# Optimization experiments

Hardware: AMD Instinct MI355X
Metric: run time of the kernel (lower is better)

Reference implementation:

```python
import jax, jax.numpy as jnp
import numpy as np

D_MODEL = 128
DEPTH = 4
LN_EPS = 1e-5


def _ssm(x, Wi, A, Wo):
    # x: [B, L, D]; Wi: [3D, D]; A: [D]; Wo: [D, D]
    z = jnp.einsum('bld,ed->ble', x, Wi)          # [B, L, 3D]
    u, i, o = jnp.split(z, 3, axis=-1)
    iu = jax.nn.sigmoid(i) * jnp.tanh(u)          # gated input, [B, L, D]
    og = jax.nn.sigmoid(o)                        # output gate
    a = jnp.minimum(jnp.exp(A), 0.999)            # decay, [D]

    def step(s, c):
        s = a * s + c
        return s, s

    s0 = jnp.zeros((x.shape[0], x.shape[2]), x.dtype)
    _, S = jax.lax.scan(step, s0, jnp.swapaxes(iu, 0, 1))  # [L, B, D]
    y = og * jnp.swapaxes(S, 0, 1)                # [B, L, D]
    return jnp.einsum('bld,ed->ble', y, Wo)


def _scan_2d(x, Wi, A, Wo):
    # x: [N, D, H, W] -> four directional 1D scans, averaged
    N, D, H, W = x.shape
    xh = jnp.transpose(x, (0, 2, 3, 1))           # [N, H, W, D]
    lr = _ssm(xh.reshape(N * H, W, D), Wi, A, Wo).reshape(N, H, W, D)
    rl = _ssm(jnp.flip(xh, 2).reshape(N * H, W, D), Wi, A, Wo).reshape(N, H, W, D)
    rl = jnp.flip(rl, 2)
    xw = jnp.transpose(x, (0, 3, 2, 1))           # [N, W, H, D]
    ud = _ssm(xw.reshape(N * W, H, D), Wi, A, Wo).reshape(N, W, H, D)
    du = _ssm(jnp.flip(xw, 2).reshape(N * W, H, D), Wi, A, Wo).reshape(N, W, H, D)
    du = jnp.flip(du, 2)
    y = (lr + rl + jnp.transpose(ud, (0, 2, 1, 3)) + jnp.transpose(du, (0, 2, 1, 3))) / 4
    return jnp.transpose(y, (0, 3, 1, 2))         # [N, D, H, W]


def setup_inputs() -> dict:
    key = jax.random.key(0)
    ks = jax.random.split(key, 8)
    D = D_MODEL
    lin = 1.0 / np.sqrt(D)
    tok = jax.random.normal(ks[0], (8, 16, D, 32, 32), jnp.float32)
    s_inp = jax.random.normal(ks[1], (DEPTH, 3 * D, D), jnp.float32) * lin
    s_A = jax.random.normal(ks[2], (DEPTH, D), jnp.float32) * -0.1
    s_out = jax.random.normal(ks[3], (DEPTH, D, D), jnp.float32) * lin
    t_inp = jax.random.normal(ks[4], (DEPTH, 3 * D, D), jnp.float32) * lin
    t_A = jax.random.normal(ks[5], (DEPTH, D), jnp.float32) * -0.1
    t_out = jax.random.normal(ks[6], (DEPTH, D, D), jnp.float32) * lin
    ln_g = jnp.ones((D,), jnp.float32)
    ln_b = jnp.zeros((D,), jnp.float32)
    return {"tok": tok, "s_inp": s_inp, "s_A": s_A, "s_out": s_out,
            "t_inp": t_inp, "t_A": t_A, "t_out": t_out,
            "ln_g": ln_g, "ln_b": ln_b}


def reference(tok, s_inp, s_A, s_out, t_inp, t_A, t_out, ln_g, ln_b):
    B, T, D, h, w = tok.shape
    x = tok
    for l in range(DEPTH):
        xs = x.reshape(B * T, D, h, w)
        xs = _scan_2d(xs, s_inp[l], s_A[l], s_out[l]).reshape(B, T, D, h, w)
        xt = jnp.transpose(xs, (0, 3, 4, 1, 2)).reshape(B * h * w, T, D)
        xt = _ssm(xt, t_inp[l], t_A[l], t_out[l]).reshape(B, h, w, T, D)
        x = x + jnp.transpose(xt, (0, 3, 4, 1, 2))
    xn = jnp.transpose(x, (0, 1, 3, 4, 2))        # [B,T,h,w,D]
    mu = jnp.mean(xn, axis=-1, keepdims=True)
    var = jnp.var(xn, axis=-1, keepdims=True)
    xn = (xn - mu) / jnp.sqrt(var + LN_EPS) * ln_g + ln_b
    return jnp.transpose(xn, (0, 1, 4, 2, 3))     # [B,T,D,h,w]
```

## Files before the change

kernel.cpp:

```cpp
#include <hip/hip_runtime.h>
#include <hip/hip_bf16.h>
#include <math.h>

#define D_MODEL 128
#define HW      1024
#define DEPTH   4
#define NIMG    128
#define B_      8
#define T_      16
#define LN_EPSF 1e-5f
#define TLN     131072
#define PS      1033

typedef short  s8  __attribute__((ext_vector_type(8)));
typedef ushort us8 __attribute__((ext_vector_type(8)));
typedef ushort us4 __attribute__((ext_vector_type(4)));
typedef float  f4  __attribute__((ext_vector_type(4)));

#define MFMA __builtin_amdgcn_mfma_f32_16x16x32_bf16

__device__ __forceinline__ float sig_(float x) { return 1.0f / (1.0f + __expf(-x)); }
__device__ __forceinline__ float tanh_(float x) { return 2.0f * sig_(2.0f * x) - 1.0f; }
__device__ __forceinline__ ushort f2b(float f) {
    __hip_bfloat16 h = __float2bfloat16(f);
    return *reinterpret_cast<ushort*>(&h);
}
__device__ __forceinline__ float b2f(ushort u) {
    __hip_bfloat16 h = *reinterpret_cast<__hip_bfloat16*>(&u);
    return __bfloat162float(h);
}

__global__ __launch_bounds__(256) void wconv_kernel(
    const float* __restrict__ src, ushort* __restrict__ dst, int n)
{
    int i = blockIdx.x * 256 + threadIdx.x;
    if (i < n) dst[i] = f2b(src[i]);
}

__device__ __forceinline__ void gates_from_lds_TL(
    const ushort (*Xs)[136], const ushort* __restrict__ Wi,
    ushort* __restrict__ iu, ushort* __restrict__ og,
    size_t nbase, int q0, int tid)
{
    const int lane = tid & 63, wv = tid >> 6, grp = lane >> 4, lrow = lane & 15;
    const int ch0 = wv * 32;

    {
        f4 aU[2][4], aI[2][4];
        #pragma unroll
        for (int nt = 0; nt < 2; ++nt)
            #pragma unroll
            for (int qt = 0; qt < 4; ++qt) { aU[nt][qt] = (f4)0.f; aI[nt][qt] = (f4)0.f; }

        #pragma unroll
        for (int kk = 0; kk < 4; ++kk) {
            const int kb = kk * 32 + grp * 8;
            s8 xb[4], wu[2], wi[2];
            #pragma unroll
            for (int qt = 0; qt < 4; ++qt)
                xb[qt] = *reinterpret_cast<const s8*>(&Xs[qt * 16 + lrow][kb]);
            #pragma unroll
            for (int nt = 0; nt < 2; ++nt) {
                const int e = ch0 + nt * 16 + lrow;
                wu[nt] = *reinterpret_cast<const s8*>(Wi + (size_t)e * D_MODEL + kb);
                wi[nt] = *reinterpret_cast<const s8*>(Wi + (size_t)(e + 128) * D_MODEL + kb);
            }
            #pragma unroll
            for (int nt = 0; nt < 2; ++nt)
                #pragma unroll
                for (int qt = 0; qt < 4; ++qt) {
                    aU[nt][qt] = MFMA(wu[nt], xb[qt], aU[nt][qt], 0, 0, 0);
                    aI[nt][qt] = MFMA(wi[nt], xb[qt], aI[nt][qt], 0, 0, 0);
                }
        }
        #pragma unroll
        for (int nt = 0; nt < 2; ++nt)
            #pragma unroll
            for (int qt = 0; qt < 4; ++qt) {
                const int ch = ch0 + nt * 16 + grp * 4;
                const int q  = q0 + qt * 16 + lrow;
                const size_t off = nbase + (size_t)(ch >> 3) * 8192 + (size_t)q * 8 + (ch & 7);
                us4 piu;
                #pragma unroll
                for (int i = 0; i < 4; ++i)
                    piu[i] = f2b(sig_(aI[nt][qt][i]) * tanh_(aU[nt][qt][i]));
                *reinterpret_cast<us4*>(iu + off) = piu;
            }
    }

    {
        f4 aO[2][4];
        #pragma unroll
        for (int nt = 0; nt < 2; ++nt)
            #pragma unroll
            for (int qt = 0; qt < 4; ++qt) aO[nt][qt] = (f4)0.f;

        #pragma unroll
        for (int kk = 0; kk < 4; ++kk) {
            const int kb = kk * 32 + grp * 8;
            s8 xb[4], wo[2];
            #pragma unroll
            for (int qt = 0; qt < 4; ++qt)
                xb[qt] = *reinterpret_cast<const s8*>(&Xs[qt * 16 + lrow][kb]);
            #pragma unroll
            for (int nt = 0; nt < 2; ++nt)
                wo[nt] = *reinterpret_cast<const s8*>(Wi + (size_t)(ch0 + nt * 16 + lrow + 256) * D_MODEL + kb);
            #pragma unroll
            for (int nt = 0; nt < 2; ++nt)
                #pragma unroll
                for (int qt = 0; qt < 4; ++qt)
                    aO[nt][qt] = MFMA(wo[nt], xb[qt], aO[nt][qt], 0, 0, 0);
        }
        #pragma unroll
        for (int nt = 0; nt < 2; ++nt)
            #pragma unroll
            for (int qt = 0; qt < 4; ++qt) {
                const int ch = ch0 + nt * 16 + grp * 4;
                const int q  = q0 + qt * 16 + lrow;
                const size_t off = nbase + (size_t)(ch >> 3) * 8192 + (size_t)q * 8 + (ch & 7);
                us4 pog;
                #pragma unroll
                for (int i = 0; i < 4; ++i)
                    pog[i] = f2b(sig_(aO[nt][qt][i]));
                *reinterpret_cast<us4*>(og + off) = pog;
            }
    }
}

__global__ __launch_bounds__(256, 3) void gates_f32_kernel(
    const float* __restrict__ in, const ushort* __restrict__ Wi,
    ushort* __restrict__ iu, ushort* __restrict__ og)
{
    __shared__ ushort Xs[64][136];
    const int n   = blockIdx.x >> 4;
    const int q0  = (blockIdx.x & 15) << 6;
    const int tid = threadIdx.x;
    const size_t nbase = (size_t)n * TLN;

    {
        const float* inb = in + nbase + q0;
        const int q = tid & 63, dh0 = tid >> 6;
        for (int it = 0; it < 4; ++it) {
            const int dh = dh0 + it * 4;
            s8 pk;
            #pragma unroll
            for (int j = 0; j < 8; ++j)
                pk[j] = (short)f2b(inb[(size_t)(dh * 8 + j) * HW + q]);
            *reinterpret_cast<s8*>(&Xs[q][dh * 8]) = pk;
        }
    }
    __syncthreads();
    gates_from_lds_TL(Xs, Wi, iu, og, nbase, q0, tid);
}

__global__ __launch_bounds__(256, 2) void scan2d_kernel(
    ushort* bufG , const ushort* __restrict__ og,
    const float* __restrict__ Av)
{
    __shared__ float P[8 * PS];
    __shared__ float R[8 * PS];
    const int n   = blockIdx.x >> 4;
    const int oct = blockIdx.x & 15;
    const int tid = threadIdx.x;
    const size_t base = (size_t)n * TLN + (size_t)oct * 8192;

    for (int it = 0; it < 4; ++it) {
        const int p  = it * 256 + tid;
        const int sw = p ^ (((p >> 5) & 7) << 2);
        us8 v = *reinterpret_cast<const us8*>(bufG + base + (size_t)p * 8);
        #pragma unroll
        for (int dc = 0; dc < 8; ++dc) P[dc * PS + sw] = b2f(v[dc]);
    }
    __syncthreads();

    const int dc  = tid & 7;
    const int row = tid >> 3;
    const float a = fminf(__expf(Av[oct * 8 + dc]), 0.999f);

    {
        const int swb = (row * 32) ^ (((row & 7) << 2));
        float x[32], r[32];
        #pragma unroll
        for (int j = 0; j < 32; ++j) x[j] = P[dc * PS + (swb ^ j)];
        float s = 0.f;
        #pragma unroll
        for (int j = 0; j < 32; ++j) { s = fmaf(a, s, x[j]); r[j] = s; }
        s = 0.f;
        #pragma unroll
        for (int j = 31; j >= 0; --j) { s = fmaf(a, s, x[j]); r[j] += s; }
        #pragma unroll
        for (int j = 0; j < 32; ++j) R[dc * PS + (swb ^ j)] = r[j];
    }
    __syncthreads();

    {
        float x[32], t[32];
        #pragma unroll
        for (int i = 0; i < 32; ++i) {
            const int p = i * 32 + row;
            x[i] = P[dc * PS + (p ^ ((i & 7) << 2))];
        }
        float s = 0.f;
        #pragma unroll
        for (int i = 0; i < 32; ++i) { s = fmaf(a, s, x[i]); t[i] = s; }
        s = 0.f;
        #pragma unroll
        for (int i = 31; i >= 0; --i) { s = fmaf(a, s, x[i]); t[i] += s; }
        #pragma unroll
        for (int i = 0; i < 32; ++i) {
            const int idx = dc * PS + ((i * 32 + row) ^ ((i & 7) << 2));
            P[idx] = t[i] + R[idx];
        }
    }
    __syncthreads();

    for (int it = 0; it < 4; ++it) {
        const int p  = it * 256 + tid;
        const int sw = p ^ (((p >> 5) & 7) << 2);
        us8 o = *reinterpret_cast<const us8*>(og + base + (size_t)p * 8);
        us8 w;
        #pragma unroll
        for (int d2 = 0; d2 < 8; ++d2)
            w[d2] = f2b(b2f(o[d2]) * P[d2 * PS + sw] * 0.25f);
        *reinterpret_cast<us8*>(bufG + base + (size_t)p * 8) = w;
    }
}

__global__ __launch_bounds__(256, 3) void fusedA_kernel(
    ushort* bufA , ushort* bufB ,
    const ushort* __restrict__ WoS, const ushort* __restrict__ WiT)
{
    __shared__ ushort Xs[64][136];
    const int n   = blockIdx.x >> 4;
    const int q0  = (blockIdx.x & 15) << 6;
    const int tid = threadIdx.x;
    const int lane = tid & 63, wv = tid >> 6, grp = lane >> 4, lrow = lane & 15;
    const size_t nbase = (size_t)n * TLN;
    const int qq = q0 + wv * 16 + lrow;

    s8 gf[4];
    #pragma unroll
    for (int kk = 0; kk < 4; ++kk)
        gf[kk] = *reinterpret_cast<const s8*>(
            bufA + nbase + (size_t)(kk * 4 + grp) * 8192 + (size_t)qq * 8);

    f4 C[8];
    #pragma unroll
    for (int et = 0; et < 8; ++et) C[et] = (f4)0.f;
    #pragma unroll
    for (int kk = 0; kk < 4; ++kk) {
        const int kb = kk * 32 + grp * 8;
        #pragma unroll
        for (int et = 0; et < 8; ++et) {
            s8 wf = *reinterpret_cast<const s8*>(WoS + (size_t)(et * 16 + lrow) * D_MODEL + kb);
            C[et] = MFMA(gf[kk], wf, C[et], 0, 0, 0);
        }
    }

    #pragma unroll
    for (int et = 0; et < 8; ++et)
        #pragma unroll
        for (int i = 0; i < 4; ++i)
            Xs[wv * 16 + grp * 4 + i][et * 16 + lrow] = f2b(C[et][i]);
    __syncthreads();

    gates_from_lds_TL(Xs, WiT, bufA, bufB, nbase, q0, tid);
}

__global__ __launch_bounds__(256) void tscan_kernel(
    ushort* __restrict__ buf, const float* __restrict__ Av)
{
    const int tid = blockIdx.x * 256 + threadIdx.x;
    const int q   = tid & 1023;
    const int oct = (tid >> 10) & 15;
    const int b   = tid >> 14;
    float aa[8], st[8];
    #pragma unroll
    for (int jj = 0; jj < 8; ++jj) {
        aa[jj] = fminf(__expf(Av[oct * 8 + jj]), 0.999f);
        st[jj] = 0.f;
    }
    const size_t base = (size_t)(b * T_) * TLN + (size_t)oct * 8192 + (size_t)q * 8;
    #pragma unroll
    for (int t = 0; t < T_; ++t) {
        ushort* p = buf + base + (size_t)t * TLN;
        us8 v = *reinterpret_cast<us8*>(p);
        us8 w;
        #pragma unroll
        for (int jj = 0; jj < 8; ++jj) {
            st[jj] = fmaf(aa[jj], st[jj], b2f(v[jj]));
            w[jj] = f2b(st[jj]);
        }
        *reinterpret_cast<us8*>(p) = w;
    }
}

template <bool GATES, bool LN>
__global__ __launch_bounds__(256, 3) void fusedB_kernel(
    ushort* bufA , ushort* bufB ,
    const ushort* __restrict__ WoT, const float* __restrict__ resid,
    float* __restrict__ X, const ushort* __restrict__ WiS2,
    const float* __restrict__ lng, const float* __restrict__ lnb)
{
    __shared__ ushort Xs[64][136];
    const int n   = blockIdx.x >> 4;
    const int q0  = (blockIdx.x & 15) << 6;
    const int tid = threadIdx.x;
    const int lane = tid & 63, wv = tid >> 6, grp = lane >> 4, lrow = lane & 15;
    const size_t nbase = (size_t)n * TLN;
    const int qq = q0 + wv * 16 + lrow;

    s8 g[4];
    #pragma unroll
    for (int kk = 0; kk < 4; ++kk) {
        const size_t off = nbase + (size_t)(kk * 4 + grp) * 8192 + (size_t)qq * 8;
        us8 sv = *reinterpret_cast<const us8*>(bufA + off);
        us8 ov = *reinterpret_cast<const us8*>(bufB + off);
        s8 gg;
        #pragma unroll
        for (int j = 0; j < 8; ++j)
            gg[j] = (short)f2b(b2f(sv[j]) * b2f(ov[j]));
        g[kk] = gg;
    }

    f4 C[8];
    #pragma unroll
    for (int et = 0; et < 8; ++et) C[et] = (f4)0.f;
    #pragma unroll
    for (int kk = 0; kk < 4; ++kk) {
        const int kb = kk * 32 + grp * 8;
        #pragma unroll
        for (int et = 0; et < 8; ++et) {
            s8 wf = *reinterpret_cast<const s8*>(WoT + (size_t)(et * 16 + lrow) * D_MODEL + kb);
            C[et] = MFMA(g[kk], wf, C[et], 0, 0, 0);
        }
    }

    const int qb = q0 + wv * 16 + grp * 4;

    #pragma unroll
    for (int et = 0; et < 8; ++et) {
        const int e = et * 16 + lrow;
        const size_t offR = nbase + (size_t)e * HW + qb;
        f4 r = *reinterpret_cast<const f4*>(resid + offR);
        #pragma unroll
        for (int i = 0; i < 4; ++i) C[et][i] += r[i];
    }

    if constexpr (LN) {
        float s4[4] = {0.f,0.f,0.f,0.f}, q4[4] = {0.f,0.f,0.f,0.f};
        #pragma unroll
        for (int et = 0; et < 8; ++et)
            #pragma unroll
            for (int i = 0; i < 4; ++i) {
                s4[i] += C[et][i];
                q4[i] += C[et][i] * C[et][i];
            }
        #pragma unroll
        for (int m = 1; m <= 8; m <<= 1)
            #pragma unroll
            for (int i = 0; i < 4; ++i) {
                s4[i] += __shfl_xor(s4[i], m);
                q4[i] += __shfl_xor(q4[i], m);
            }
        float mean[4], rstd[4];
        #pragma unroll
        for (int i = 0; i < 4; ++i) {
            mean[i] = s4[i] * (1.f / D_MODEL);
            rstd[i] = rsqrtf(q4[i] * (1.f / D_MODEL) - mean[i] * mean[i] + LN_EPSF);
        }
        #pragma unroll
        for (int et = 0; et < 8; ++et) {
            const int e = et * 16 + lrow;
            const float ge = lng[e], be = lnb[e];
            const size_t offX = nbase + (size_t)e * HW + qb;
            f4 o;
            #pragma unroll
            for (int i = 0; i < 4; ++i)
                o[i] = (C[et][i] - mean[i]) * rstd[i] * ge + be;
            *reinterpret_cast<f4*>(X + offX) = o;
        }
    } else {
        #pragma unroll
        for (int et = 0; et < 8; ++et) {
            const int e = et * 16 + lrow;
            const size_t offX = nbase + (size_t)e * HW + qb;
            f4 v;
            #pragma unroll
            for (int i = 0; i < 4; ++i) v[i] = C[et][i];
            *reinterpret_cast<f4*>(X + offX) = v;
            if constexpr (GATES) {
                #pragma unroll
                for (int i = 0; i < 4; ++i)
                    Xs[wv * 16 + grp * 4 + i][e] = f2b(v[i]);
            }
        }
        if constexpr (GATES) {
            __syncthreads();
            gates_from_lds_TL(Xs, WiS2, bufA, bufB, nbase, q0, tid);
        }
    }
}

extern "C" void kernel_launch(void* const* d_in, const int* in_sizes, int n_in,
                              void* d_out, int out_size, void* d_ws, size_t ws_size,
                              hipStream_t stream) {
    const float* tok   = (const float*)d_in[0];
    const float* s_inp = (const float*)d_in[1];
    const float* s_A   = (const float*)d_in[2];
    const float* s_out = (const float*)d_in[3];
    const float* t_inp = (const float*)d_in[4];
    const float* t_A   = (const float*)d_in[5];
    const float* t_out = (const float*)d_in[6];
    const float* ln_g  = (const float*)d_in[7];
    const float* ln_b  = (const float*)d_in[8];

    float*  X    = (float*)d_out;
    ushort* Abuf = (ushort*)d_ws;
    ushort* Bbuf = Abuf + (size_t)16777216;
    ushort* Wbf  = Bbuf + (size_t)16777216;
    ushort* sWiB = Wbf;
    ushort* sWoB = Wbf + 196608;
    ushort* tWiB = Wbf + 262144;
    ushort* tWoB = Wbf + 458752;

    const dim3 blk256(256);

    wconv_kernel<<<768, blk256, 0, stream>>>(s_inp, sWiB, 196608);
    wconv_kernel<<<256, blk256, 0, stream>>>(s_out, sWoB, 65536);
    wconv_kernel<<<768, blk256, 0, stream>>>(t_inp, tWiB, 196608);
    wconv_kernel<<<256, blk256, 0, stream>>>(t_out, tWoB, 65536);

    gates_f32_kernel<<<2048, blk256, 0, stream>>>(tok, sWiB, Abuf, Bbuf);

    for (int l = 0; l < DEPTH; ++l) {
        const float* xin = (l == 0) ? tok : X;

        scan2d_kernel<<<2048, blk256, 0, stream>>>(Abuf, Bbuf, s_A + (size_t)l * 128);
        fusedA_kernel<<<2048, blk256, 0, stream>>>(
            Abuf, Bbuf, sWoB + (size_t)l * 16384, tWiB + (size_t)l * 49152);
        tscan_kernel<<<512, blk256, 0, stream>>>(Abuf, t_A + (size_t)l * 128);

        if (l < DEPTH - 1) {
            fusedB_kernel<true, false><<<2048, blk256, 0, stream>>>(
                Abuf, Bbuf, tWoB + (size_t)l * 16384, xin, X,
                sWiB + (size_t)(l + 1) * 49152, nullptr, nullptr);
        } else {
            fusedB_kernel<false, true><<<2048, blk256, 0, stream>>>(
                Abuf, Bbuf, tWoB + (size_t)l * 16384, xin, X,
                nullptr, ln_g, ln_b);
        }
    }
}
```

Measured before the change: 764.3 us.

## Switch intermediate gate buffers from channel-octet to channel-major layout

Changes the bf16 intermediate buffers from an [oct][q][8] interleaved layout to plain channel-major [D][HW]. All producers and consumers (gate GEMMs, 2D scan, time scan, fused output kernels) are rewritten to transpose through LDS with the new indexing, and the MFMA operand order is swapped to match. The scan kernel now prefetches the output gate before filling LDS, and the fused-B kernel is split into a residual-plus-gates version and a separate layernorm version. The aim is more contiguous global accesses and simpler time-scan addressing. The cost is extra LDS transposes, with possible bank conflicts on column-wise writes.

Result: faster. 683.1 us, median of 2 (-10.6%).

```diff
diff --git a/kernel.cpp b/kernel.cpp
--- a/kernel.cpp
+++ b/kernel.cpp
@@ -37,7 +37,7 @@
     if (i < n) dst[i] = f2b(src[i]);
 }
 
-__device__ __forceinline__ void gates_from_lds_TL(
+__device__ __forceinline__ void gates_from_lds(
     const ushort (*Xs)[136], const ushort* __restrict__ Wi,
     ushort* __restrict__ iu, ushort* __restrict__ og,
     size_t nbase, int q0, int tid)
@@ -46,19 +46,19 @@
     const int ch0 = wv * 32;
 
     {
-        f4 aU[2][4], aI[2][4];
-        #pragma unroll
-        for (int nt = 0; nt < 2; ++nt)
-            #pragma unroll
-            for (int qt = 0; qt < 4; ++qt) { aU[nt][qt] = (f4)0.f; aI[nt][qt] = (f4)0.f; }
+        f4 aU[4][2], aI[4][2];
+        #pragma unroll
+        for (int mt = 0; mt < 4; ++mt)
+            #pragma unroll
+            for (int nt = 0; nt < 2; ++nt) { aU[mt][nt] = (f4)0.f; aI[mt][nt] = (f4)0.f; }
 
         #pragma unroll
         for (int kk = 0; kk < 4; ++kk) {
             const int kb = kk * 32 + grp * 8;
-            s8 xb[4], wu[2], wi[2];
-            #pragma unroll
-            for (int qt = 0; qt < 4; ++qt)
-                xb[qt] = *reinterpret_cast<const s8*>(&Xs[qt * 16 + lrow][kb]);
+            s8 xa[4], wu[2], wi[2];
+            #pragma unroll
+            for (int mt = 0; mt < 4; ++mt)
+                xa[mt] = *reinterpret_cast<const s8*>(&Xs[mt * 16 + lrow][kb]);
             #pragma unroll
             for (int nt = 0; nt < 2; ++nt) {
                 const int e = ch0 + nt * 16 + lrow;
@@ -66,62 +66,59 @@
                 wi[nt] = *reinterpret_cast<const s8*>(Wi + (size_t)(e + 128) * D_MODEL + kb);
             }
             #pragma unroll
-            for (int nt = 0; nt < 2; ++nt)
+            for (int mt = 0; mt < 4; ++mt)
                 #pragma unroll
-                for (int qt = 0; qt < 4; ++qt) {
-                    aU[nt][qt] = MFMA(wu[nt], xb[qt], aU[nt][qt], 0, 0, 0);
-                    aI[nt][qt] = MFMA(wi[nt], xb[qt], aI[nt][qt], 0, 0, 0);
+                for (int nt = 0; nt < 2; ++nt) {
+                    aU[mt][nt] = MFMA(xa[mt], wu[nt], aU[mt][nt], 0, 0, 0);
+                    aI[mt][nt] = MFMA(xa[mt], wi[nt], aI[mt][nt], 0, 0, 0);
                 }
         }
         #pragma unroll
-        for (int nt = 0; nt < 2; ++nt)
-            #pragma unroll
-            for (int qt = 0; qt < 4; ++qt) {
-                const int ch = ch0 + nt * 16 + grp * 4;
-                const int q  = q0 + qt * 16 + lrow;
-                const size_t off = nbase + (size_t)(ch >> 3) * 8192 + (size_t)q * 8 + (ch & 7);
+        for (int mt = 0; mt < 4; ++mt)
+            #pragma unroll
+            for (int nt = 0; nt < 2; ++nt) {
+                const int e = ch0 + nt * 16 + lrow;
+                const size_t off = nbase + (size_t)e * HW + q0 + mt * 16 + grp * 4;
                 us4 piu;
                 #pragma unroll
                 for (int i = 0; i < 4; ++i)
-                    piu[i] = f2b(sig_(aI[nt][qt][i]) * tanh_(aU[nt][qt][i]));
+                    piu[i] = f2b(sig_(aI[mt][nt][i]) * tanh_(aU[mt][nt][i]));
                 *reinterpret_cast<us4*>(iu + off) = piu;
             }
     }
-
     {
-        f4 aO[2][4];
-        #pragma unroll
-        for (int nt = 0; nt < 2; ++nt)
-            #pragma unroll
-            for (int qt = 0; qt < 4; ++qt) aO[nt][qt] = (f4)0.f;
+        f4 aO[4][2];
+        #pragma unroll
+        for (int mt = 0; mt < 4; ++mt)
+            #pragma unroll
+            for (int nt = 0; nt < 2; ++nt) aO[mt][nt] = (f4)0.f;
 
         #pragma unroll
         for (int kk = 0; kk < 4; ++kk) {
             const int kb = kk * 32 + grp * 8;
-            s8 xb[4], wo[2];
-            #pragma unroll
-            for (int qt = 0; qt < 4; ++qt)
-                xb[qt] = *reinterpret_cast<const s8*>(&Xs[qt * 16 + lrow][kb]);
+            s8 xa[4], wo[2];
+            #pragma unroll
+            for (int mt = 0; mt < 4; ++mt)
+                xa[mt] = *reinterpret_cast<const s8*>(&Xs[mt * 16 + lrow][kb]);
             #pragma unroll
             for (int nt = 0; nt < 2; ++nt)
                 wo[nt] = *reinterpret_cast<const s8*>(Wi + (size_t)(ch0 + nt * 16 + lrow + 256) * D_MODEL + kb);
             #pragma unroll
-            for (int nt = 0; nt < 2; ++nt)
+            for (int mt = 0; mt < 4; ++mt)
                 #pragma unroll
-                for (int qt = 0; qt < 4; ++qt)
-                    aO[nt][qt] = MFMA(wo[nt], xb[qt], aO[nt][qt], 0, 0, 0);
-        }
-        #pragma unroll
-        for (int nt = 0; nt < 2; ++nt)
-            #pragma unroll
-            for (int qt = 0; qt < 4; ++qt) {
-                const int ch = ch0 + nt * 16 + grp * 4;
-                const int q  = q0 + qt * 16 + lrow;
-                const size_t off = nbase + (size_t)(ch >> 3) * 8192 + (size_t)q * 8 + (ch & 7);
+                for (int nt = 0; nt < 2; ++nt)
+                    aO[mt][nt] = MFMA(xa[mt], wo[nt], aO[mt][nt], 0, 0, 0);
+        }
+        #pragma unroll
+        for (int mt = 0; mt < 4; ++mt)
+            #pragma unroll
+            for (int nt = 0; nt < 2; ++nt) {
+                const int e = ch0 + nt * 16 + lrow;
+                const size_t off = nbase + (size_t)e * HW + q0 + mt * 16 + grp * 4;
                 us4 pog;
                 #pragma unroll
                 for (int i = 0; i < 4; ++i)
-                    pog[i] = f2b(sig_(aO[nt][qt][i]));
+                    pog[i] = f2b(sig_(aO[mt][nt][i]));
                 *reinterpret_cast<us4*>(og + off) = pog;
             }
     }
@@ -137,20 +134,17 @@
     const int tid = threadIdx.x;
     const size_t nbase = (size_t)n * TLN;
 
-    {
-        const float* inb = in + nbase + q0;
-        const int q = tid & 63, dh0 = tid >> 6;
-        for (int it = 0; it < 4; ++it) {
-            const int dh = dh0 + it * 4;
-            s8 pk;
-            #pragma unroll
-            for (int j = 0; j < 8; ++j)
-                pk[j] = (short)f2b(inb[(size_t)(dh * 8 + j) * HW + q]);
-            *reinterpret_cast<s8*>(&Xs[q][dh * 8]) = pk;
-        }
-    }
-    __syncthreads();
-    gates_from_lds_TL(Xs, Wi, iu, og, nbase, q0, tid);
+    #pragma unroll
+    for (int it = 0; it < 8; ++it) {
+        const int c  = it * 256 + tid;
+        const int ch = c >> 4;
+        const int qo = c & 15;
+        f4 v = *reinterpret_cast<const f4*>(in + nbase + (size_t)ch * HW + q0 + qo * 4);
+        #pragma unroll
+        for (int j = 0; j < 4; ++j) Xs[qo * 4 + j][ch] = f2b(v[j]);
+    }
+    __syncthreads();
+    gates_from_lds(Xs, Wi, iu, og, nbase, q0, tid);
 }
 
 __global__ __launch_bounds__(256, 2) void scan2d_kernel(
@@ -162,14 +156,26 @@
     const int n   = blockIdx.x >> 4;
     const int oct = blockIdx.x & 15;
     const int tid = threadIdx.x;
-    const size_t base = (size_t)n * TLN + (size_t)oct * 8192;
-
+    const size_t base = (size_t)n * TLN + (size_t)(oct * 8) * HW;
+
+    us8 ogv[4];
+    #pragma unroll
     for (int it = 0; it < 4; ++it) {
-        const int p  = it * 256 + tid;
-        const int sw = p ^ (((p >> 5) & 7) << 2);
-        us8 v = *reinterpret_cast<const us8*>(bufG + base + (size_t)p * 8);
-        #pragma unroll
-        for (int dc = 0; dc < 8; ++dc) P[dc * PS + sw] = b2f(v[dc]);
+        const int c  = it * 256 + tid;
+        const int dc = c >> 7, po = c & 127;
+        ogv[it] = *reinterpret_cast<const us8*>(og + base + (size_t)dc * HW + po * 8);
+    }
+
+    #pragma unroll
+    for (int it = 0; it < 4; ++it) {
+        const int c  = it * 256 + tid;
+        const int dc = c >> 7, po = c & 127;
+        us8 v = *reinterpret_cast<const us8*>(bufG + base + (size_t)dc * HW + po * 8);
+        #pragma unroll
+        for (int j = 0; j < 8; ++j) {
+            const int p = po * 8 + j;
+            P[dc * PS + (p ^ (((p >> 5) & 7) << 2))] = b2f(v[j]);
+        }
     }
     __syncthreads();
 
@@ -178,7 +184,7 @@
     const float a = fminf(__expf(Av[oct * 8 + dc]), 0.999f);
 
     {
-        const int swb = (row * 32) ^ (((row & 7) << 2));
+        const int swb = (row * 32) ^ ((row & 7) << 2);
         float x[32], r[32];
         #pragma unroll
         for (int j = 0; j < 32; ++j) x[j] = P[dc * PS + (swb ^ j)];
@@ -214,15 +220,17 @@
     }
     __syncthreads();
 
+    #pragma unroll
     for (int it = 0; it < 4; ++it) {
-        const int p  = it * 256 + tid;
-        const int sw = p ^ (((p >> 5) & 7) << 2);
-        us8 o = *reinterpret_cast<const us8*>(og + base + (size_t)p * 8);
+        const int c  = it * 256 + tid;
+        const int dc2 = c >> 7, po = c & 127;
         us8 w;
         #pragma unroll
-        for (int d2 = 0; d2 < 8; ++d2)
-            w[d2] = f2b(b2f(o[d2]) * P[d2 * PS + sw] * 0.25f);
-        *reinterpret_cast<us8*>(bufG + base + (size_t)p * 8) = w;
+        for (int j = 0; j < 8; ++j) {
+            const int p = po * 8 + j;
+            w[j] = f2b(b2f(ogv[it][j]) * P[dc2 * PS + (p ^ (((p >> 5) & 7) << 2))] * 0.25f);
+        }
+        *reinterpret_cast<us8*>(bufG + base + (size_t)dc2 * HW + po * 8) = w;
     }
 }
 
@@ -230,19 +238,194 @@
     ushort* bufA , ushort* bufB ,
     const ushort* __restrict__ WoS, const ushort* __restrict__ WiT)
 {
-    __shared__ ushort Xs[64][136];
+    __shared__ ushort Gs[64][136];
+    const int n   = blockIdx.x >> 4;
+    const int q0  = (blockIdx.x & 15) << 6;
+    const int tid = threadIdx.x;
+    const int lane = tid & 63, wv = tid >> 6, grp = lane >> 4, lrow = lane & 15;
+    const int ch0 = wv * 32;
+    const size_t nbase = (size_t)n * TLN;
+
+    #pragma unroll
+    for (int it = 0; it < 4; ++it) {
+        const int c  = it * 256 + tid;
+        const int ch = c >> 3, qo = c & 7;
+        us8 v = *reinterpret_cast<const us8*>(bufA + nbase + (size_t)ch * HW + q0 + qo * 8);
+        #pragma unroll
+        for (int j = 0; j < 8; ++j) Gs[qo * 8 + j][ch] = v[j];
+    }
+    __syncthreads();
+
+    f4 c1[2][4];
+    #pragma unroll
+    for (int et = 0; et < 2; ++et)
+        #pragma unroll
+        for (int qt = 0; qt < 4; ++qt) c1[et][qt] = (f4)0.f;
+
+    #pragma unroll
+    for (int kk = 0; kk < 4; ++kk) {
+        const int kb = kk * 32 + grp * 8;
+        s8 wf[2], xg[4];
+        #pragma unroll
+        for (int et = 0; et < 2; ++et)
+            wf[et] = *reinterpret_cast<const s8*>(WoS + (size_t)(ch0 + et * 16 + lrow) * D_MODEL + kb);
+        #pragma unroll
+        for (int qt = 0; qt < 4; ++qt)
+            xg[qt] = *reinterpret_cast<const s8*>(&Gs[qt * 16 + lrow][kb]);
+        #pragma unroll
+        for (int et = 0; et < 2; ++et)
+            #pragma unroll
+            for (int qt = 0; qt < 4; ++qt)
+                c1[et][qt] = MFMA(wf[et], xg[qt], c1[et][qt], 0, 0, 0);
+    }
+    __syncthreads();
+
+    #pragma unroll
+    for (int et = 0; et < 2; ++et)
+        #pragma unroll
+        for (int qt = 0; qt < 4; ++qt) {
+            us4 pk;
+            #pragma unroll
+            for (int i = 0; i < 4; ++i) pk[i] = f2b(c1[et][qt][i]);
+            *reinterpret_cast<us4*>(&Gs[qt * 16 + lrow][ch0 + et * 16 + grp * 4]) = pk;
+        }
+    __syncthreads();
+
+    gates_from_lds(Gs, WiT, bufA, bufB, nbase, q0, tid);
+}
+
+__global__ __launch_bounds__(256) void tscan_kernel(
+    ushort* __restrict__ buf, const float* __restrict__ Av)
+{
+    const int tid = blockIdx.x * 256 + threadIdx.x;
+    const int qo = tid & 127;
+    const int d  = (tid >> 7) & 127;
+    const int b  = tid >> 14;
+    const float a = fminf(__expf(Av[d]), 0.999f);
+    const size_t base = (size_t)(b * T_) * TLN + (size_t)d * HW + qo * 8;
+    float st[8];
+    #pragma unroll
+    for (int j = 0; j < 8; ++j) st[j] = 0.f;
+    #pragma unroll
+    for (int t = 0; t < T_; ++t) {
+        ushort* p = buf + base + (size_t)t * TLN;
+        us8 v = *reinterpret_cast<us8*>(p);
+        us8 w;
+        #pragma unroll
+        for (int j = 0; j < 8; ++j) {
+            st[j] = fmaf(a, st[j], b2f(v[j]));
+            w[j] = f2b(st[j]);
+        }
+        *reinterpret_cast<us8*>(p) = w;
+    }
+}
+
+__global__ __launch_bounds__(256, 3) void fusedB_kernel(
+    ushort* bufA , ushort* bufB ,
+    const ushort* __restrict__ WoT, const float* __restrict__ resid,
+    float* __restrict__ X, const ushort* __restrict__ WiS2)
+{
+    __shared__ ushort Gs[64][136];
+    const int n   = blockIdx.x >> 4;
+    const int q0  = (blockIdx.x & 15) << 6;
+    const int tid = threadIdx.x;
+    const int lane = tid & 63, wv = tid >> 6, grp = lane >> 4, lrow = lane & 15;
+    const int ch0 = wv * 32;
+    const size_t nbase = (size_t)n * TLN;
+
+    #pragma unroll
+    for (int it = 0; it < 4; ++it) {
+        const int c  = it * 256 + tid;
+        const int ch = c >> 3, qo = c & 7;
+        const size_t o = nbase + (size_t)ch * HW + q0 + qo * 8;
+        us8 sv = *reinterpret_cast<const us8*>(bufA + o);
+        us8 ov = *reinterpret_cast<const us8*>(bufB + o);
+        #pragma unroll
+        for (int j = 0; j < 8; ++j) Gs[qo * 8 + j][ch] = f2b(b2f(sv[j]) * b2f(ov[j]));
+    }
+
+    f4 r[4][2];
+    #pragma unroll
+    for (int mt = 0; mt < 4; ++mt)
+        #pragma unroll
+        for (int nt = 0; nt < 2; ++nt)
+            r[mt][nt] = *reinterpret_cast<const f4*>(
+                resid + nbase + (size_t)(ch0 + nt * 16 + lrow) * HW + q0 + mt * 16 + grp * 4);
+    __syncthreads();
+
+    f4 C[4][2];
+    #pragma unroll
+    for (int mt = 0; mt < 4; ++mt)
+        #pragma unroll
+        for (int nt = 0; nt < 2; ++nt) C[mt][nt] = (f4)0.f;
+
+    #pragma unroll
+    for (int kk = 0; kk < 4; ++kk) {
+        const int kb = kk * 32 + grp * 8;
+        s8 xg[4], wf[2];
+        #pragma unroll
+        for (int mt = 0; mt < 4; ++mt)
+            xg[mt] = *reinterpret_cast<const s8*>(&Gs[mt * 16 + lrow][kb]);
+        #pragma unroll
+        for (int nt = 0; nt < 2; ++nt)
+            wf[nt] = *reinterpret_cast<const s8*>(WoT + (size_t)(ch0 + nt * 16 + lrow) * D_MODEL + kb);
+        #pragma unroll
+        for (int mt = 0; mt < 4; ++mt)
+            #pragma unroll
+            for (int nt = 0; nt < 2; ++nt)
+                C[mt][nt] = MFMA(xg[mt], wf[nt], C[mt][nt], 0, 0, 0);
+    }
+    __syncthreads();
+
+    #pragma unroll
+    for (int mt = 0; mt < 4; ++mt)
+        #pragma unroll
+        for (int nt = 0; nt < 2; ++nt) {
+            const int e    = ch0 + nt * 16 + lrow;
+            const int qloc = mt * 16 + grp * 4;
+            const size_t off = nbase + (size_t)e * HW + q0 + qloc;
+            f4 v;
+            #pragma unroll
+            for (int i = 0; i < 4; ++i) v[i] = C[mt][nt][i] + r[mt][nt][i];
+            *reinterpret_cast<f4*>(X + off) = v;
+            #pragma unroll
+            for (int i = 0; i < 4; ++i) Gs[qloc + i][e] = f2b(v[i]);
+        }
+    __syncthreads();
+    gates_from_lds(Gs, WiS2, bufA, bufB, nbase, q0, tid);
+}
+
+__global__ __launch_bounds__(256, 3) void fusedB_ln_kernel(
+    const ushort* __restrict__ bufA, const ushort* __restrict__ bufB,
+    const ushort* __restrict__ WoT, const float* __restrict__ resid,
+    float* __restrict__ X,
+    const float* __restrict__ lng, const float* __restrict__ lnb)
+{
+    __shared__ ushort Gs[64][136];
     const int n   = blockIdx.x >> 4;
     const int q0  = (blockIdx.x & 15) << 6;
     const int tid = threadIdx.x;
     const int lane = tid & 63, wv = tid >> 6, grp = lane >> 4, lrow = lane & 15;
     const size_t nbase = (size_t)n * TLN;
-    const int qq = q0 + wv * 16 + lrow;
-
-    s8 gf[4];
-    #pragma unroll
-    for (int kk = 0; kk < 4; ++kk)
-        gf[kk] = *reinterpret_cast<const s8*>(
-            bufA + nbase + (size_t)(kk * 4 + grp) * 8192 + (size_t)qq * 8);
+
+    #pragma unroll
+    for (int it = 0; it < 4; ++it) {
+        const int c  = it * 256 + tid;
+        const int ch = c >> 3, qo = c & 7;
+        const size_t o = nbase + (size_t)ch * HW + q0 + qo * 8;
+        us8 sv = *reinterpret_cast<const us8*>(bufA + o);
+        us8 ov = *reinterpret_cast<const us8*>(bufB + o);
+        #pragma unroll
+        for (int j = 0; j < 8; ++j) Gs[qo * 8 + j][ch] = f2b(b2f(sv[j]) * b2f(ov[j]));
+    }
+
+    const int qb = q0 + wv * 16 + grp * 4;
+    f4 r[8];
+    #pragma unroll
+    for (int et = 0; et < 8; ++et)
+        r[et] = *reinterpret_cast<const f4*>(
+            resid + nbase + (size_t)(et * 16 + lrow) * HW + qb);
+    __syncthreads();
 
     f4 C[8];
     #pragma unroll
@@ -250,155 +433,46 @@
     #pragma unroll
     for (int kk = 0; kk < 4; ++kk) {
         const int kb = kk * 32 + grp * 8;
-        #pragma unroll
-        for (int et = 0; et < 8; ++et) {
-            s8 wf = *reinterpret_cast<const s8*>(WoS + (size_t)(et * 16 + lrow) * D_MODEL + kb);
-            C[et] = MFMA(gf[kk], wf, C[et], 0, 0, 0);
-        }
-    }
-
-    #pragma unroll
-    for (int et = 0; et < 8; ++et)
-        #pragma unroll
-        for (int i = 0; i < 4; ++i)
-            Xs[wv * 16 + grp * 4 + i][et * 16 + lrow] = f2b(C[et][i]);
-    __syncthreads();
-
-    gates_from_lds_TL(Xs, WiT, bufA, bufB, nbase, q0, tid);
-}
-
-__global__ __launch_bounds__(256) void tscan_kernel(
-    ushort* __restrict__ buf, const float* __restrict__ Av)
-{
-    const int tid = blockIdx.x * 256 + threadIdx.x;
-    const int q   = tid & 1023;
-    const int oct = (tid >> 10) & 15;
-    const int b   = tid >> 14;
-    float aa[8], st[8];
-    #pragma unroll
-    for (int jj = 0; jj < 8; ++jj) {
-        aa[jj] = fminf(__expf(Av[oct * 8 + jj]), 0.999f);
-        st[jj] = 0.f;
-    }
-    const size_t base = (size_t)(b * T_) * TLN + (size_t)oct * 8192 + (size_t)q * 8;
-    #pragma unroll
-    for (int t = 0; t < T_; ++t) {
-        ushort* p = buf + base + (size_t)t * TLN;
-        us8 v = *reinterpret_cast<us8*>(p);
-        us8 w;
-        #pragma unroll
-        for (int jj = 0; jj < 8; ++jj) {
-            st[jj] = fmaf(aa[jj], st[jj], b2f(v[jj]));
-            w[jj] = f2b(st[jj]);
-        }
-        *reinterpret_cast<us8*>(p) = w;
-    }
-}
-
-template <bool GATES, bool LN>
-__global__ __launch_bounds__(256, 3) void fusedB_kernel(
-    ushort* bufA , ushort* bufB ,
-    const ushort* __restrict__ WoT, const float* __restrict__ resid,
-    float* __restrict__ X, const ushort* __restrict__ WiS2,
-    const float* __restrict__ lng, const float* __restrict__ lnb)
-{
-    __shared__ ushort Xs[64][136];
-    const int n   = blockIdx.x >> 4;
-    const int q0  = (blockIdx.x & 15) << 6;
-    const int tid = threadIdx.x;
-    const int lane = tid & 63, wv = tid >> 6, grp = lane >> 4, lrow = lane & 15;
-    const size_t nbase = (size_t)n * TLN;
-    const int qq = q0 + wv * 16 + lrow;
-
-    s8 g[4];
-    #pragma unroll
-    for (int kk = 0; kk < 4; ++kk) {
-        const size_t off = nbase + (size_t)(kk * 4 + grp) * 8192 + (size_t)qq * 8;
-        us8 sv = *reinterpret_cast<const us8*>(bufA + off);
-        us8 ov = *reinterpret_cast<const us8*>(bufB + off);
-        s8 gg;
-        #pragma unroll
-        for (int j = 0; j < 8; ++j)
-            gg[j] = (short)f2b(b2f(sv[j]) * b2f(ov[j]));
-        g[kk] = gg;
-    }
-
-    f4 C[8];
-    #pragma unroll
-    for (int et = 0; et < 8; ++et) C[et] = (f4)0.f;
-    #pragma unroll
-    for (int kk = 0; kk < 4; ++kk) {
-        const int kb = kk * 32 + grp * 8;
+        s8 xa = *reinterpret_cast<const s8*>(&Gs[wv * 16 + lrow][kb]);
         #pragma unroll
         for (int et = 0; et < 8; ++et) {
             s8 wf = *reinterpret_cast<const s8*>(WoT + (size_t)(et * 16 + lrow) * D_MODEL + kb);
-            C[et] = MFMA(g[kk], wf, C[et], 0, 0, 0);
-        }
-    }
-
-    const int qb = q0 + wv * 16 + grp * 4;
-
+            C[et] = MFMA(xa, wf, C[et], 0, 0, 0);
+        }
+    }
+
+    float s4[4] = {0.f,0.f,0.f,0.f}, q4[4] = {0.f,0.f,0.f,0.f};
+    #pragma unroll
+    for (int et = 0; et < 8; ++et)
+        #pragma unroll
+        for (int i = 0; i < 4; ++i) {
+            const float v = C[et][i] + r[et][i];
+            C[et][i] = v;
+            s4[i] += v; q4[i] += v * v;
+        }
+    #pragma unroll
+    for (int m = 1; m <= 8; m <<= 1)
+        #pragma unroll
+        for (int i = 0; i < 4; ++i) {
+            s4[i] += __shfl_xor(s4[i], m);
+            q4[i] += __shfl_xor(q4[i], m);
+        }
+    float mean[4], rstd[4];
+    #pragma unroll
+    for (int i = 0; i < 4; ++i) {
+        mean[i] = s4[i] * (1.f / D_MODEL);
+        rstd[i] = rsqrtf(q4[i] * (1.f / D_MODEL) - mean[i] * mean[i] + LN_EPSF);
+    }
     #pragma unroll
     for (int et = 0; et < 8; ++et) {
         const int e = et * 16 + lrow;
-        const size_t offR = nbase + (size_t)e * HW + qb;
-        f4 r = *reinterpret_cast<const f4*>(resid + offR);
-        #pragma unroll
-        for (int i = 0; i < 4; ++i) C[et][i] += r[i];
-    }
-
-    if constexpr (LN) {
-        float s4[4] = {0.f,0.f,0.f,0.f}, q4[4] = {0.f,0.f,0.f,0.f};
-        #pragma unroll
-        for (int et = 0; et < 8; ++et)
-            #pragma unroll
-            for (int i = 0; i < 4; ++i) {
-                s4[i] += C[et][i];
-                q4[i] += C[et][i] * C[et][i];
-            }
-        #pragma unroll
-        for (int m = 1; m <= 8; m <<= 1)
-            #pragma unroll
-            for (int i = 0; i < 4; ++i) {
-                s4[i] += __shfl_xor(s4[i], m);
-                q4[i] += __shfl_xor(q4[i], m);
-            }
-        float mean[4], rstd[4];
-        #pragma unroll
-        for (int i = 0; i < 4; ++i) {
-            mean[i] = s4[i] * (1.f / D_MODEL);
-            rstd[i] = rsqrtf(q4[i] * (1.f / D_MODEL) - mean[i] * mean[i] + LN_EPSF);
-        }
-        #pragma unroll
-        for (int et = 0; et < 8; ++et) {
-            const int e = et * 16 + lrow;
-            const float ge = lng[e], be = lnb[e];
-            const size_t offX = nbase + (size_t)e * HW + qb;
-            f4 o;
-            #pragma unroll
-            for (int i = 0; i < 4; ++i)
-                o[i] = (C[et][i] - mean[i]) * rstd[i] * ge + be;
-            *reinterpret_cast<f4*>(X + offX) = o;
-        }
-    } else {
-        #pragma unroll
-        for (int et = 0; et < 8; ++et) {
-            const int e = et * 16 + lrow;
-            const size_t offX = nbase + (size_t)e * HW + qb;
-            f4 v;
-            #pragma unroll
-            for (int i = 0; i < 4; ++i) v[i] = C[et][i];
-            *reinterpret_cast<f4*>(X + offX) = v;
-            if constexpr (GATES) {
-                #pragma unroll
-                for (int i = 0; i < 4; ++i)
-                    Xs[wv * 16 + grp * 4 + i][e] = f2b(v[i]);
-            }
-        }
-        if constexpr (GATES) {
-            __syncthreads();
-            gates_from_lds_TL(Xs, WiS2, bufA, bufB, nbase, q0, tid);
-        }
+        const float ge = lng[e], be = lnb[e];
+        const size_t off = nbase + (size_t)e * HW + qb;
+        f4 o;
+        #pragma unroll
+        for (int i = 0; i < 4; ++i)
+            o[i] = (C[et][i] - mean[i]) * rstd[i] * ge + be;
+        *reinterpret_cast<f4*>(X + off) = o;
     }
 }
 
@@ -442,13 +516,12 @@
         tscan_kernel<<<512, blk256, 0, stream>>>(Abuf, t_A + (size_t)l * 128);
 
         if (l < DEPTH - 1) {
-            fusedB_kernel<true, false><<<2048, blk256, 0, stream>>>(
+            fusedB_kernel<<<2048, blk256, 0, stream>>>(
                 Abuf, Bbuf, tWoB + (size_t)l * 16384, xin, X,
-                sWiB + (size_t)(l + 1) * 49152, nullptr, nullptr);
+                sWiB + (size_t)(l + 1) * 49152);
         } else {
-            fusedB_kernel<false, true><<<2048, blk256, 0, stream>>>(
-                Abuf, Bbuf, tWoB + (size_t)l * 16384, xin, X,
-                nullptr, ln_g, ln_b);
-        }
-    }
-}
+            fusedB_ln_kernel<<<2048, blk256, 0, stream>>>(
+                Abuf, Bbuf, tWoB + (size_t)l * 16384, xin, X, ln_g, ln_b);
+        }
+    }
+}
```
